# Kernel tuning notes

Measured on AMD Instinct MI355X. Metric: run time of the kernel, lower is better.

Reference implementation:

```python
import jax, jax.numpy as jnp
import numpy as np

TEMPERATURE = 11.313708498984761  # sqrt(128)


def setup_inputs() -> dict:
    key = jax.random.key(0)
    kq, kk, kv = jax.random.split(key, 3)
    b, n, m, d, dv = 16, 2048, 2048, 128, 128
    return {
        "queries": jax.random.normal(kq, (b, n, d), dtype=jnp.float32),
        "keys": jax.random.normal(kk, (b, m, d), dtype=jnp.float32),
        "values": jax.random.normal(kv, (b, m, dv), dtype=jnp.float32),
    }


def reference(queries, keys, values):
    # scores: [b, n, m]
    scores = jnp.einsum('bnd,bmd->bnm', queries, keys) / TEMPERATURE
    attn = jax.nn.softmax(scores, axis=2)
    # out: [b, n, d']
    return jnp.einsum('bnm,bmd->bnd', attn, values)
```

## Files before the change

### kernel.cpp

```cpp
#include <hip/hip_runtime.h>


#define BATCH 16
#define SEQ   2048
#define DIM   128
#define NT    (SEQ / 64)

typedef short bf16x8 __attribute__((ext_vector_type(8)));
typedef float f32x16 __attribute__((ext_vector_type(16)));

static __device__ __forceinline__ unsigned pk2(float lo, float hi) {
  union { float f; unsigned u; } a, b;
  a.f = lo; b.f = hi;
  return ((b.u + 0x8000u) & 0xffff0000u) | ((a.u + 0x8000u) >> 16);
}
static __device__ __forceinline__ float fast_exp2(float x) {
#if __has_builtin(__builtin_amdgcn_exp2f)
  return __builtin_amdgcn_exp2f(x);
#else
  return exp2f(x);
#endif
}

typedef __attribute__((address_space(1))) const unsigned int g_u32;
typedef __attribute__((address_space(3))) unsigned int l_u32;
static __device__ __forceinline__ void gl2lds16(const unsigned short* g, unsigned short* l) {
  __builtin_amdgcn_global_load_lds((g_u32*)g, (l_u32*)l, 16, 0, 0);
}

__global__ __launch_bounds__(256)
void prep_kernel(const float* __restrict__ K, const float* __restrict__ V,
                 unsigned short* __restrict__ Kb, unsigned short* __restrict__ Vt,
                 float scale) {
  const int bx = blockIdx.x, tid = threadIdx.x;
  if (bx < 2048) {
    size_t idx = (size_t)bx * 256 + tid;
    const float4* kf = (const float4*)K;
    float4 a = kf[idx * 2], c = kf[idx * 2 + 1];
    uint4 o;
    o.x = pk2(a.x * scale, a.y * scale);
    o.y = pk2(a.z * scale, a.w * scale);
    o.z = pk2(c.x * scale, c.y * scale);
    o.w = pk2(c.z * scale, c.w * scale);
    ((uint4*)Kb)[idx] = o;
  } else {
    __shared__ float tile[128][33];
    const int vb = bx - 2048;
    const int b = vb >> 6, r = vb & 63;
    const int m0 = (r & 15) * 128, d0 = (r >> 4) * 32;
    const int c = tid & 7, mr = tid >> 3;
    const float* src = V + ((size_t)(b * SEQ) + m0) * DIM + d0;
#pragma unroll
    for (int it = 0; it < 4; ++it) {
      int m = it * 32 + mr;
      float4 x = *(const float4*)(src + (size_t)m * DIM + c * 4);
      tile[m][c * 4 + 0] = x.x; tile[m][c * 4 + 1] = x.y;
      tile[m][c * 4 + 2] = x.z; tile[m][c * 4 + 3] = x.w;
    }
    __syncthreads();
    const int dr = tid >> 3, s = tid & 7;
    unsigned short* dst = Vt + ((size_t)(b * DIM) + d0 + dr) * SEQ + m0;
#pragma unroll
    for (int it = 0; it < 2; ++it) {
      int slot = it * 8 + s;
      uint4 o;
      o.x = pk2(tile[slot * 8 + 0][dr], tile[slot * 8 + 1][dr]);
      o.y = pk2(tile[slot * 8 + 2][dr], tile[slot * 8 + 3][dr]);
      o.z = pk2(tile[slot * 8 + 4][dr], tile[slot * 8 + 5][dr]);
      o.w = pk2(tile[slot * 8 + 6][dr], tile[slot * 8 + 7][dr]);
      *(uint4*)(dst + slot * 8) = o;
    }
  }
}


__global__ __launch_bounds__(256, 2)
void attn_kernel(const float* __restrict__ Qf,
                 const unsigned short* __restrict__ Kb,
                 const unsigned short* __restrict__ Vtb,
                 float* __restrict__ out) {
  __shared__ __align__(1024) unsigned char smem[65536];
  unsigned short* sm16 = (unsigned short*)smem;

  const int tid  = threadIdx.x;
  const int wv   = tid >> 6;
  const int w_q  = wv & 1;
  const int w_m  = wv >> 1;
  const int lane = tid & 63;
  const int l31  = lane & 31;
  const int q2   = lane >> 5;
  const int b    = blockIdx.x;
  const int q0   = blockIdx.y * 64 + w_q * 32;

  const unsigned short* kb = Kb  + (size_t)b * SEQ * DIM;
  const unsigned short* vb = Vtb + (size_t)b * SEQ * DIM;

  bf16x8 aq[8];
  {
    const float* qp = Qf + ((size_t)(b * SEQ) + q0 + l31) * DIM + q2 * 8;
#pragma unroll
    for (int c = 0; c < 8; ++c) {
      float4 x = *(const float4*)(qp + c * 16);
      float4 y = *(const float4*)(qp + c * 16 + 4);
      union { unsigned i[4]; bf16x8 v; } u;
      u.i[0] = pk2(x.x, x.y); u.i[1] = pk2(x.z, x.w);
      u.i[2] = pk2(y.x, y.y); u.i[3] = pk2(y.z, y.w);
      aq[c] = u.v;
    }
  }

  unsigned kgo[4], vgo[4];
#pragma unroll
  for (int i = 0; i < 4; ++i) {
    int ch = wv * 4 + i;
    int krow = ch * 4 + (lane >> 4);
    kgo[i] = (unsigned)(krow * 128) + ((((lane & 15) << 4) ^ ((krow & 15) << 4)) >> 1);
    int vrow = ch * 8 + (lane >> 3);
    vgo[i] = (unsigned)(vrow * 2048) + ((((lane & 7) << 4) ^ ((vrow & 7) << 4)) >> 1);
  }

  const int kro = ((w_m * 32 + l31) << 8) + ((q2 << 4) ^ ((l31 & 15) << 4));
  const int vro = (l31 << 7) + (((w_m << 6) + (q2 << 4)) ^ ((l31 & 7) << 4));

  f32x16 oacc[4];
#pragma unroll
  for (int t = 0; t < 4; ++t)
#pragma unroll
    for (int i = 0; i < 16; ++i) oacc[t][i] = 0.0f;
  float ls[4] = {0.0f, 0.0f, 0.0f, 0.0f};

#define STAGE(TK, BUF) do {                                                  \
    const unsigned short* kt_b = kb + ((size_t)(TK) << 13);                  \
    const unsigned short* vt_b = vb + ((TK) << 6);                           \
    unsigned short* kd = sm16 + (((BUF) + wv * 4096) >> 1);                  \
    unsigned short* vd = sm16 + ((32768 + (BUF) + wv * 4096) >> 1);          \
    _Pragma("unroll")                                                        \
    for (int i = 0; i < 4; ++i) gl2lds16(kt_b + kgo[i], kd + i * 512);       \
    _Pragma("unroll")                                                        \
    for (int i = 0; i < 4; ++i) gl2lds16(vt_b + vgo[i], vd + i * 512);       \
  } while (0)

  STAGE(0, 0);

  for (int kt = 0; kt < NT; ++kt) {
    const int cur = (kt & 1) << 14;
    __syncthreads();
    if (kt + 1 < NT) STAGE(kt + 1, 16384 - cur);

    const unsigned char* kB = smem + cur;
    const unsigned char* vB = smem + 32768 + cur;

    f32x16 se, so;
#pragma unroll
    for (int i = 0; i < 16; ++i) { se[i] = 0.0f; so[i] = 0.0f; }
    __builtin_amdgcn_s_setprio(1);
#pragma unroll
    for (int c = 0; c < 4; ++c) {
      bf16x8 b0 = *(const bf16x8*)(kB + (kro ^ ((2 * c) << 5)));
      se = __builtin_amdgcn_mfma_f32_32x32x16_bf16(b0, aq[2 * c], se, 0, 0, 0);
      bf16x8 b1 = *(const bf16x8*)(kB + (kro ^ ((2 * c + 1) << 5)));
      so = __builtin_amdgcn_mfma_f32_32x32x16_bf16(b1, aq[2 * c + 1], so, 0, 0, 0);
    }
    __builtin_amdgcn_s_setprio(0);

    float p[16];
#pragma unroll
    for (int i = 0; i < 16; ++i) p[i] = fast_exp2(se[i] + so[i]);
#pragma unroll
    for (int i = 0; i < 4; ++i) {
      ls[0] += p[4 * i + 0]; ls[1] += p[4 * i + 1];
      ls[2] += p[4 * i + 2]; ls[3] += p[4 * i + 3];
    }

    unsigned d0, d1, d2, d3, d4, d5, d6, d7;
    asm("v_cvt_pk_bf16_f32 %0, %1, %2" : "=v"(d0) : "v"(p[0]),  "v"(p[1]));
    asm("v_cvt_pk_bf16_f32 %0, %1, %2" : "=v"(d1) : "v"(p[2]),  "v"(p[3]));
    asm("v_cvt_pk_bf16_f32 %0, %1, %2" : "=v"(d2) : "v"(p[4]),  "v"(p[5]));
    asm("v_cvt_pk_bf16_f32 %0, %1, %2" : "=v"(d3) : "v"(p[6]),  "v"(p[7]));
    asm("v_cvt_pk_bf16_f32 %0, %1, %2" : "=v"(d4) : "v"(p[8]),  "v"(p[9]));
    asm("v_cvt_pk_bf16_f32 %0, %1, %2" : "=v"(d5) : "v"(p[10]), "v"(p[11]));
    asm("v_cvt_pk_bf16_f32 %0, %1, %2" : "=v"(d6) : "v"(p[12]), "v"(p[13]));
    asm("v_cvt_pk_bf16_f32 %0, %1, %2" : "=v"(d7) : "v"(p[14]), "v"(p[15]));
    asm("v_permlane32_swap_b32 %0, %1" : "+v"(d0), "+v"(d2));
    asm("v_permlane32_swap_b32 %0, %1" : "+v"(d1), "+v"(d3));
    asm("v_permlane32_swap_b32 %0, %1" : "+v"(d4), "+v"(d6));
    asm("v_permlane32_swap_b32 %0, %1" : "+v"(d5), "+v"(d7));
    union { unsigned u[4]; bf16x8 v; } pu0, pu1;
    pu0.u[0] = d0; pu0.u[1] = d1; pu0.u[2] = d2; pu0.u[3] = d3;
    pu1.u[0] = d4; pu1.u[1] = d5; pu1.u[2] = d6; pu1.u[3] = d7;

    __builtin_amdgcn_s_setprio(1);
#pragma unroll
    for (int t = 0; t < 4; ++t) {
      bf16x8 bv0 = *(const bf16x8*)(vB + t * 4096 + vro);
      oacc[t] = __builtin_amdgcn_mfma_f32_32x32x16_bf16(pu0.v, bv0, oacc[t], 0, 0, 0);
      bf16x8 bv1 = *(const bf16x8*)(vB + t * 4096 + (vro ^ 32));
      oacc[t] = __builtin_amdgcn_mfma_f32_32x32x16_bf16(pu1.v, bv1, oacc[t], 0, 0, 0);
    }
    __builtin_amdgcn_s_setprio(0);
  }
#undef STAGE

  float lsum = (ls[0] + ls[1]) + (ls[2] + ls[3]);
  lsum += __shfl_xor(lsum, 32, 64);

  __syncthreads();
  float* cb  = (float*)smem;
  float* cbL = (float*)(smem + 32768);
  if (w_m == 1) {
    float* my = cb + w_q * 4096;
#pragma unroll
    for (int t = 0; t < 4; ++t)
#pragma unroll
      for (int r = 0; r < 16; ++r)
        my[(t * 16 + r) * 64 + lane] = oacc[t][r];
  }
  cbL[w_m * 64 + w_q * 32 + l31] = lsum;
  __syncthreads();
  if (w_m == 0) {
    const float* pr = cb + w_q * 4096;
    float linv[16];
#pragma unroll
    for (int r = 0; r < 16; ++r) {
      int qr = (r & 3) + ((r >> 2) << 3) + (q2 << 2);
      linv[r] = 1.0f / (cbL[w_q * 32 + qr] + cbL[64 + w_q * 32 + qr]);
    }
    float* ob = out + ((size_t)(b * SEQ) + q0) * DIM;
#pragma unroll
    for (int t = 0; t < 4; ++t)
#pragma unroll
      for (int r = 0; r < 16; ++r) {
        int qr = (r & 3) + ((r >> 2) << 3) + (q2 << 2);
        ob[(size_t)qr * DIM + t * 32 + l31] = (oacc[t][r] + pr[(t * 16 + r) * 64 + lane]) * linv[r];
      }
  }
}

extern "C" void kernel_launch(void* const* d_in, const int* in_sizes, int n_in,
                              void* d_out, int out_size, void* d_ws, size_t ws_size,
                              hipStream_t stream) {
  const float* Q = (const float*)d_in[0];
  const float* K = (const float*)d_in[1];
  const float* V = (const float*)d_in[2];
  float* out = (float*)d_out;

  const size_t elems = (size_t)BATCH * SEQ * DIM;
  unsigned short* Kb = (unsigned short*)d_ws;
  unsigned short* Vt = Kb + elems;

  const double TEMPERATURE = 11.313708498984761;
  const float scale = (float)(1.4426950408889634 / TEMPERATURE);

  prep_kernel<<<3072, 256, 0, stream>>>(K, V, Kb, Vt, scale);
  attn_kernel<<<dim3(BATCH, SEQ / 64), 256, 0, stream>>>(Q, Kb, Vt, out);
}
```

Measured before the change: 135.1 us.

## Split key range across four waves with per-wave private LDS and no block barriers

```diff
diff --git a/kernel.cpp b/kernel.cpp
--- a/kernel.cpp
+++ b/kernel.cpp
@@ -4,7 +4,7 @@
 #define BATCH 16
 #define SEQ   2048
 #define DIM   128
-#define NT    (SEQ / 64)
+#define NT    (SEQ / 128)
 
 typedef short bf16x8 __attribute__((ext_vector_type(8)));
 typedef float f32x16 __attribute__((ext_vector_type(16)));
@@ -79,18 +79,19 @@
                  const unsigned short* __restrict__ Kb,
                  const unsigned short* __restrict__ Vtb,
                  float* __restrict__ out) {
-  __shared__ __align__(1024) unsigned char smem[65536];
+  __shared__ __align__(1024) unsigned char smem[66560];
   unsigned short* sm16 = (unsigned short*)smem;
 
   const int tid  = threadIdx.x;
   const int wv   = tid >> 6;
-  const int w_q  = wv & 1;
-  const int w_m  = wv >> 1;
   const int lane = tid & 63;
   const int l31  = lane & 31;
   const int q2   = lane >> 5;
-  const int b    = blockIdx.x;
-  const int q0   = blockIdx.y * 64 + w_q * 32;
+
+  const int f  = blockIdx.x;
+  const int w  = ((f & 7) << 7) + (f >> 3);
+  const int b  = w >> 6;
+  const int q0 = (w & 63) << 5;
 
   const unsigned short* kb = Kb  + (size_t)b * SEQ * DIM;
   const unsigned short* vb = Vtb + (size_t)b * SEQ * DIM;
@@ -109,18 +110,29 @@
     }
   }
 
-  unsigned kgo[4], vgo[4];
-#pragma unroll
-  for (int i = 0; i < 4; ++i) {
-    int ch = wv * 4 + i;
-    int krow = ch * 4 + (lane >> 4);
-    kgo[i] = (unsigned)(krow * 128) + ((((lane & 15) << 4) ^ ((krow & 15) << 4)) >> 1);
-    int vrow = ch * 8 + (lane >> 3);
-    vgo[i] = (unsigned)(vrow * 2048) + ((((lane & 7) << 4) ^ ((vrow & 7) << 4)) >> 1);
-  }
-
-  const int kro = ((w_m * 32 + l31) << 8) + ((q2 << 4) ^ ((l31 & 15) << 4));
-  const int vro = (l31 << 7) + (((w_m << 6) + (q2 << 4)) ^ ((l31 & 7) << 4));
+  unsigned koff[8], voff[8];
+#pragma unroll
+  for (int i = 0; i < 8; ++i) {
+    int r = i * 4 + (lane >> 4);
+    koff[i] = (unsigned)((wv * 32 + r) * 128 + (((lane & 15) ^ (r & 15)) << 3));
+    int dv = i * 16 + (lane >> 2);
+    voff[i] = (unsigned)(dv * 2048 + wv * 32 + (((lane & 3) ^ (dv & 3)) << 3));
+  }
+  unsigned short* kd = sm16 + wv * 8192;
+  unsigned short* vd = sm16 + wv * 8192 + 4096;
+  const unsigned char* kS = smem + wv * 16384;
+  const unsigned char* vS = smem + wv * 16384 + 8192;
+
+#define STAGE_K(TK) do {                                                     \
+    const unsigned short* s_ = kb + ((size_t)(TK) << 14);                    \
+    _Pragma("unroll")                                                        \
+    for (int i = 0; i < 8; ++i) gl2lds16(s_ + koff[i], kd + i * 512);        \
+  } while (0)
+#define STAGE_V(TK) do {                                                     \
+    const unsigned short* s_ = vb + ((TK) << 7);                             \
+    _Pragma("unroll")                                                        \
+    for (int i = 0; i < 8; ++i) gl2lds16(s_ + voff[i], vd + i * 512);        \
+  } while (0)
 
   f32x16 oacc[4];
 #pragma unroll
@@ -129,26 +141,21 @@
     for (int i = 0; i < 16; ++i) oacc[t][i] = 0.0f;
   float ls[4] = {0.0f, 0.0f, 0.0f, 0.0f};
 
-#define STAGE(TK, BUF) do {                                                  \
-    const unsigned short* kt_b = kb + ((size_t)(TK) << 13);                  \
-    const unsigned short* vt_b = vb + ((TK) << 6);                           \
-    unsigned short* kd = sm16 + (((BUF) + wv * 4096) >> 1);                  \
-    unsigned short* vd = sm16 + ((32768 + (BUF) + wv * 4096) >> 1);          \
-    _Pragma("unroll")                                                        \
-    for (int i = 0; i < 4; ++i) gl2lds16(kt_b + kgo[i], kd + i * 512);       \
-    _Pragma("unroll")                                                        \
-    for (int i = 0; i < 4; ++i) gl2lds16(vt_b + vgo[i], vd + i * 512);       \
-  } while (0)
-
-  STAGE(0, 0);
-
+  STAGE_K(0);
+  STAGE_V(0);
+
+#pragma unroll 1
   for (int kt = 0; kt < NT; ++kt) {
-    const int cur = (kt & 1) << 14;
-    __syncthreads();
-    if (kt + 1 < NT) STAGE(kt + 1, 16384 - cur);
-
-    const unsigned char* kB = smem + cur;
-    const unsigned char* vB = smem + 32768 + cur;
+    asm volatile("s_waitcnt vmcnt(0)" ::: "memory");
+    __builtin_amdgcn_sched_barrier(0);
+
+    bf16x8 kf[8];
+#pragma unroll
+    for (int c = 0; c < 8; ++c)
+      kf[c] = *(const bf16x8*)(kS + l31 * 256 + ((((c << 1) + q2) ^ (l31 & 15)) << 4));
+    asm volatile("s_waitcnt lgkmcnt(0)" ::: "memory");
+    __builtin_amdgcn_sched_barrier(0);
+    if (kt + 1 < NT) STAGE_K(kt + 1);
 
     f32x16 se, so;
 #pragma unroll
@@ -156,10 +163,8 @@
     __builtin_amdgcn_s_setprio(1);
 #pragma unroll
     for (int c = 0; c < 4; ++c) {
-      bf16x8 b0 = *(const bf16x8*)(kB + (kro ^ ((2 * c) << 5)));
-      se = __builtin_amdgcn_mfma_f32_32x32x16_bf16(b0, aq[2 * c], se, 0, 0, 0);
-      bf16x8 b1 = *(const bf16x8*)(kB + (kro ^ ((2 * c + 1) << 5)));
-      so = __builtin_amdgcn_mfma_f32_32x32x16_bf16(b1, aq[2 * c + 1], so, 0, 0, 0);
+      se = __builtin_amdgcn_mfma_f32_32x32x16_bf16(kf[2 * c],     aq[2 * c],     se, 0, 0, 0);
+      so = __builtin_amdgcn_mfma_f32_32x32x16_bf16(kf[2 * c + 1], aq[2 * c + 1], so, 0, 0, 0);
     }
     __builtin_amdgcn_s_setprio(0);
 
@@ -192,47 +197,54 @@
     __builtin_amdgcn_s_setprio(1);
 #pragma unroll
     for (int t = 0; t < 4; ++t) {
-      bf16x8 bv0 = *(const bf16x8*)(vB + t * 4096 + vro);
+      int row = t * 32 + l31;
+      bf16x8 bv0 = *(const bf16x8*)(vS + row * 64 + (((q2 << 4)) ^ ((row & 3) << 4)));
       oacc[t] = __builtin_amdgcn_mfma_f32_32x32x16_bf16(pu0.v, bv0, oacc[t], 0, 0, 0);
-      bf16x8 bv1 = *(const bf16x8*)(vB + t * 4096 + (vro ^ 32));
+      bf16x8 bv1 = *(const bf16x8*)(vS + row * 64 + ((32 + (q2 << 4)) ^ ((row & 3) << 4)));
       oacc[t] = __builtin_amdgcn_mfma_f32_32x32x16_bf16(pu1.v, bv1, oacc[t], 0, 0, 0);
     }
     __builtin_amdgcn_s_setprio(0);
-  }
-#undef STAGE
+
+    asm volatile("s_waitcnt lgkmcnt(0)" ::: "memory");
+    __builtin_amdgcn_sched_barrier(0);
+    if (kt + 1 < NT) STAGE_V(kt + 1);
+  }
+#undef STAGE_K
+#undef STAGE_V
 
   float lsum = (ls[0] + ls[1]) + (ls[2] + ls[3]);
   lsum += __shfl_xor(lsum, 32, 64);
 
-  __syncthreads();
-  float* cb  = (float*)smem;
-  float* cbL = (float*)(smem + 32768);
-  if (w_m == 1) {
-    float* my = cb + w_q * 4096;
-#pragma unroll
-    for (int t = 0; t < 4; ++t)
-#pragma unroll
-      for (int r = 0; r < 16; ++r)
-        my[(t * 16 + r) * 64 + lane] = oacc[t][r];
-  }
-  cbL[w_m * 64 + w_q * 32 + l31] = lsum;
-  __syncthreads();
-  if (w_m == 0) {
-    const float* pr = cb + w_q * 4096;
-    float linv[16];
+  float* myp = (float*)(smem + wv * 16384);
+#pragma unroll
+  for (int t = 0; t < 4; ++t)
 #pragma unroll
     for (int r = 0; r < 16; ++r) {
       int qr = (r & 3) + ((r >> 2) << 3) + (q2 << 2);
-      linv[r] = 1.0f / (cbL[w_q * 32 + qr] + cbL[64 + w_q * 32 + qr]);
-    }
-    float* ob = out + ((size_t)(b * SEQ) + q0) * DIM;
-#pragma unroll
-    for (int t = 0; t < 4; ++t)
-#pragma unroll
-      for (int r = 0; r < 16; ++r) {
-        int qr = (r & 3) + ((r >> 2) << 3) + (q2 << 2);
-        ob[(size_t)qr * DIM + t * 32 + l31] = (oacc[t][r] + pr[(t * 16 + r) * 64 + lane]) * linv[r];
-      }
+      myp[qr * 128 + t * 32 + l31] = oacc[t][r];
+    }
+  float* lsumL = (float*)(smem + 65536);
+  if (q2 == 0) lsumL[wv * 32 + l31] = lsum;
+  __syncthreads();
+
+  const float* ob = out + ((size_t)(b * SEQ) + q0) * DIM;
+#pragma unroll
+  for (int pass = 0; pass < 2; ++pass) {
+    int q = wv * 8 + pass * 4 + (lane >> 4);
+    float linv = 1.0f / (lsumL[q] + lsumL[32 + q] + lsumL[64 + q] + lsumL[96 + q]);
+#pragma unroll
+    for (int half = 0; half < 2; ++half) {
+      int d4 = (lane & 15) + half * 16;
+      float4 v = *(const float4*)(smem + q * 512 + d4 * 16);
+      float4 v1 = *(const float4*)(smem + 16384 + q * 512 + d4 * 16);
+      float4 v2 = *(const float4*)(smem + 32768 + q * 512 + d4 * 16);
+      float4 v3 = *(const float4*)(smem + 49152 + q * 512 + d4 * 16);
+      v.x = (v.x + v1.x + v2.x + v3.x) * linv;
+      v.y = (v.y + v1.y + v2.y + v3.y) * linv;
+      v.z = (v.z + v1.z + v2.z + v3.z) * linv;
+      v.w = (v.w + v1.w + v2.w + v3.w) * linv;
+      *(float4*)((float*)ob + (size_t)q * DIM + d4 * 4) = v;
+    }
   }
 }
 
@@ -252,5 +264,5 @@
   const float scale = (float)(1.4426950408889634 / TEMPERATURE);
 
   prep_kernel<<<3072, 256, 0, stream>>>(K, V, Kb, Vt, scale);
-  attn_kernel<<<dim3(BATCH, SEQ / 64), 256, 0, stream>>>(Q, Kb, Vt, out);
-}
+  attn_kernel<<<1024, 256, 0, stream>>>(Q, Kb, Vt, out);
+}
```

After: 149.1 us. +10.4%, slower.
